# Performance work log

Hardware: AMD Instinct MI355X
Metric: run time of the kernel (lower is better)

## Reference

```python
import jax, jax.numpy as jnp
import numpy as np

N_G, E_G = 50000, 800000
N_S, E_S = 10000, 160000
NF = 64
B = 8

def _w(key, shape):
    fan_in = shape[-1]
    return jax.random.normal(key, shape, dtype=jnp.float32) / np.sqrt(fan_in)

def setup_inputs() -> dict:
    key = jax.random.key(0)
    ks = jax.random.split(key, 40)
    inp = {
        "graph_x": jax.random.normal(ks[0], (N_G, NF), dtype=jnp.float32),
        "subgraph_x": jax.random.normal(ks[1], (N_S, NF), dtype=jnp.float32),
        "point": jax.random.normal(ks[2], (B, NF), dtype=jnp.float32),
        "graph_edge_index": jax.random.randint(ks[3], (2, E_G), 0, N_G),
        "graph_batch": jnp.sort(jax.random.randint(ks[4], (N_G,), 0, B)),
        "subgraph_edge_index": jax.random.randint(ks[5], (2, E_S), 0, N_S),
        "subgraph_batch": jnp.sort(jax.random.randint(ks[6], (N_S,), 0, B)),
    }
    # GraphConv params per branch: channel sizes 64->128->256->192
    dims = [(2 * NF, NF), (4 * NF, 2 * NF), (3 * NF, 4 * NF)]
    i = 7
    for pre in ("g", "s"):
        for li, (o, c) in enumerate(dims, start=1):
            inp[f"{pre}W{li}r"] = _w(ks[i], (o, c)); i += 1  # lin_rel (aggregated)
            inp[f"{pre}W{li}n"] = _w(ks[i], (o, c)); i += 1  # lin_root (self)
            inp[f"{pre}B{li}"] = jnp.zeros((o,), dtype=jnp.float32)
    inp["l1W"] = _w(ks[i], (600, 3 * NF + 3 * NF + NF)); i += 1
    inp["l1b"] = jnp.zeros((600,), dtype=jnp.float32)
    inp["l2W"] = _w(ks[i], (256, 600)); i += 1
    inp["l2b"] = jnp.zeros((256,), dtype=jnp.float32)
    inp["l3W"] = _w(ks[i], (NF, 256)); i += 1
    inp["l3b"] = jnp.zeros((NF,), dtype=jnp.float32)
    return inp

def _graph_conv(x, src, dst, Wr, Wn, b, n_nodes):
    # PyG GraphConv: out_i = Wr @ sum_{j->i} x_j + Wn @ x_i + b
    agg = jax.ops.segment_sum(x[src], dst, num_segments=n_nodes)
    return agg @ Wr.T + x @ Wn.T + b

def _scatter_mean(x, seg, num_segments):
    s = jax.ops.segment_sum(x, seg, num_segments=num_segments)
    cnt = jax.ops.segment_sum(jnp.ones((x.shape[0],), x.dtype), seg, num_segments=num_segments)
    return s / jnp.maximum(cnt, 1.0)[:, None]

def _branch(x, edge_index, batch, params, n_nodes):
    src, dst = edge_index[0], edge_index[1]
    for (Wr, Wn, b) in params:
        x = jax.nn.elu(_graph_conv(x, src, dst, Wr, Wn, b, n_nodes))
    return _scatter_mean(x, batch, B)

def reference(graph_x, subgraph_x, point,
              gW1r, gW1n, gB1, gW2r, gW2n, gB2, gW3r, gW3n, gB3,
              sW1r, sW1n, sB1, sW2r, sW2n, sB2, sW3r, sW3n, sB3,
              l1W, l1b, l2W, l2b, l3W, l3b,
              graph_edge_index, graph_batch, subgraph_edge_index, subgraph_batch):
    x1 = _branch(graph_x, graph_edge_index, graph_batch,
                 [(gW1r, gW1n, gB1), (gW2r, gW2n, gB2), (gW3r, gW3n, gB3)], N_G)
    x2 = _branch(subgraph_x, subgraph_edge_index, subgraph_batch,
                 [(sW1r, sW1n, sB1), (sW2r, sW2n, sB2), (sW3r, sW3n, sB3)], N_S)
    x = jnp.concatenate([x1, x2, point], axis=-1)  # [B, 448]
    x = jax.nn.relu(x @ l1W.T + l1b)
    x = jax.nn.relu(x @ l2W.T + l2b)
    return x @ l3W.T + l3b  # [B, 64]
```

## Files before the change

kernel.cpp:

```cpp
#include <hip/hip_runtime.h>
#include <cmath>

typedef __attribute__((ext_vector_type(8))) short short8;
typedef __attribute__((ext_vector_type(4))) short shortx4;
typedef __attribute__((ext_vector_type(4))) float floatx4;
typedef __attribute__((ext_vector_type(2))) float floatx2;
typedef __attribute__((ext_vector_type(4))) int intx4;
typedef __attribute__((ext_vector_type(2))) int intx2;

#define N_G 50000
#define E_G 800000
#define N_S 10000
#define E_S 160000
#define NT (N_G + N_S)
#define ET (E_G + E_S)
#define BATCH 8
#define STRIDE 64
#define FPASS 8

__device__ __forceinline__ float b2f(short s) {
    unsigned u = ((unsigned)(unsigned short)s) << 16;
    return __builtin_bit_cast(float, u);
}
__device__ __forceinline__ short f2b(float f) {
    unsigned u = __builtin_bit_cast(unsigned, f);
    u += 0x7FFF + ((u >> 16) & 1);
    return (short)(u >> 16);
}
__device__ __forceinline__ short8 fp8x8_to_bf16(intx2 w) {
    floatx2 f0 = __builtin_amdgcn_cvt_pk_f32_fp8(w[0], false);
    floatx2 f1 = __builtin_amdgcn_cvt_pk_f32_fp8(w[0], true);
    floatx2 f2 = __builtin_amdgcn_cvt_pk_f32_fp8(w[1], false);
    floatx2 f3 = __builtin_amdgcn_cvt_pk_f32_fp8(w[1], true);
    short8 r;
    r[0]=f2b(f0[0]); r[1]=f2b(f0[1]); r[2]=f2b(f1[0]); r[3]=f2b(f1[1]);
    r[4]=f2b(f2[0]); r[5]=f2b(f2[1]); r[6]=f2b(f3[0]); r[7]=f2b(f3[1]);
    return r;
}

struct RepArgs { const float* Wr[6]; const float* Wn[6]; short* dst[6]; int cin[6]; int nk[6]; int groups[6]; };
__global__ void init_kernel(const float* __restrict__ gx, const float* __restrict__ sx,
                            unsigned char* __restrict__ X0_8,
                            int* __restrict__ dcount, float* __restrict__ pooled,
                            const int* __restrict__ g_batch, const int* __restrict__ s_batch,
                            int* __restrict__ starts, RepArgs ra, int total_groups) {
    int t = blockIdx.x * blockDim.x + threadIdx.x;
    if (t < NT * 16) {
        size_t e = (size_t)t * 4;
        const float* src = (e < (size_t)N_G * 64) ? (gx + e) : (sx + (e - (size_t)N_G * 64));
        floatx4 v = *(const floatx4*)src;
        int w8 = 0;
        w8 = __builtin_amdgcn_cvt_pk_fp8_f32(v[0], v[1], w8, false);
        w8 = __builtin_amdgcn_cvt_pk_fp8_f32(v[2], v[3], w8, true);
        *(unsigned int*)(X0_8 + e) = (unsigned int)w8;
    }
    if (t < NT) dcount[t] = 0;
    if (t < 16 * 192) pooled[t] = 0.f;
    if (t <= 16) {
        int b = t;
        if (b == 16) { starts[16] = NT; }
        else {
            int key, n, base;
            const int* arr;
            if (b < 8) { arr = g_batch; n = N_G; key = b; base = 0; }
            else       { arr = s_batch; n = N_S; key = b - 8; base = N_G; }
            int lo = 0, hi = n;
            while (lo < hi) { int mid = (lo + hi) >> 1; if (arr[mid] < key) lo = mid + 1; else hi = mid; }
            starts[b] = base + lo;
        }
    }
    if (t < total_groups) {
        int seg = 0, off = t;
        while (seg < 5 && off >= ra.groups[seg]) { off -= ra.groups[seg]; ++seg; }
        int CIN = ra.cin[seg], NK = ra.nk[seg];
        int lane = off & 63;
        int rest = off >> 6;
        int tt = rest % NK;
        int ot = rest / NK;
        int o = ot * 16 + (lane & 15);
        int kk = tt * 32 + (lane >> 4) * 8;
        const float* src = (kk < CIN) ? (ra.Wr[seg] + (size_t)o * CIN + kk)
                                      : (ra.Wn[seg] + (size_t)o * CIN + (kk - CIN));
        floatx4 u0 = *(const floatx4*)src;
        floatx4 u1 = *(const floatx4*)(src + 4);
        short8 d;
        d[0]=f2b(u0[0]); d[1]=f2b(u0[1]); d[2]=f2b(u0[2]); d[3]=f2b(u0[3]);
        d[4]=f2b(u1[0]); d[5]=f2b(u1[1]); d[6]=f2b(u1[2]); d[7]=f2b(u1[3]);
        *(short8*)(ra.dst[seg] + (size_t)off * 8) = d;
    }
}

__global__ void fill_kernel(const int* __restrict__ g_ei, const int* __restrict__ s_ei,
                            int* __restrict__ dcount, int* __restrict__ csr) {
    int pass = blockIdx.x & (FPASS - 1);
    int lb   = blockIdx.x >> 3;
    int t = lb * blockDim.x + threadIdx.x;
    if (t >= ET) return;
    int dst;
    if (t < E_G) dst = g_ei[E_G + t];
    else         dst = s_ei[E_S + (t - E_G)] + N_G;
    int lo = pass * (NT / FPASS);
    int hi = lo + (NT / FPASS);
    if (dst < lo || dst >= hi) return;
    int src;
    if (t < E_G) src = g_ei[t];
    else         src = s_ei[t - E_G] + N_G;
    int slot = atomicAdd(&dcount[dst], 1);
    if (slot < STRIDE) csr[(size_t)dst * STRIDE + slot] = src;
}

template<int C>
__global__ void agg8_kernel(const unsigned char* __restrict__ x8, const int* __restrict__ dcount,
                            const int* __restrict__ csr, short* __restrict__ out) {
    constexpr int C16 = C / 16;
    int t = blockIdx.x * blockDim.x + threadIdx.x;
    if (t >= NT * C16) return;
    int node = t / C16;
    int ch   = t % C16;
    int e0 = node * STRIDE;
    int e1 = e0 + min(dcount[node], STRIDE);
    float acc[16];
    #pragma unroll
    for (int j = 0; j < 16; ++j) acc[j] = 0.f;
    for (int e = e0; e < e1; ++e) {
        int s = csr[e];
        intx4 w = *(const intx4*)(x8 + (size_t)s * C + ch * 16);
        #pragma unroll
        for (int q = 0; q < 4; ++q) {
            floatx2 f0 = __builtin_amdgcn_cvt_pk_f32_fp8(w[q], false);
            floatx2 f1 = __builtin_amdgcn_cvt_pk_f32_fp8(w[q], true);
            acc[q * 4 + 0] += f0[0];
            acc[q * 4 + 1] += f0[1];
            acc[q * 4 + 2] += f1[0];
            acc[q * 4 + 3] += f1[1];
        }
    }
    short8 o0, o1;
    #pragma unroll
    for (int j = 0; j < 8; ++j) { o0[j] = f2b(acc[j]); o1[j] = f2b(acc[8 + j]); }
    short8* q = (short8*)(out + (size_t)node * C + ch * 16);
    q[0] = o0; q[1] = o1;
}

template<int CIN, int COUT, bool POOL>
__global__ __launch_bounds__(256) void gemm_elu_kernel(
        const short* __restrict__ A1, const unsigned char* __restrict__ A2_8,
        const short* __restrict__ gWF, const short* __restrict__ sWF,
        const float* __restrict__ gB, const float* __restrict__ sB,
        unsigned char* __restrict__ out8,
        float* __restrict__ pooled, const int* __restrict__ starts) {
    constexpr int NK  = CIN / 16;
    constexpr int NOT = COUT / 16;
    constexpr int TILE_SH = NK * 512;
    constexpr int MAX_SH = 16384;
    constexpr int CHUNK_OT = (NOT * TILE_SH <= MAX_SH) ? NOT : (MAX_SH / TILE_SH);
    static_assert(NOT % CHUNK_OT == 0, "chunk must divide NOT");
    constexpr int CH_SH = CHUNK_OT * TILE_SH;
    __shared__ short lds[CH_SH];

    int wave = threadIdx.x >> 6;
    int lane = threadIdx.x & 63;
    int tile0 = blockIdx.x << 2;
    int myTile = tile0 + wave;
    bool active = myTile < (NT / 16);
    int tileC = active ? myTile : (NT / 16 - 1);
    int r0 = tileC * 16;
    bool sub = (r0 >= N_G);
    const short* WF = sub ? sWF : gWF;
    const float* bias = sub ? sB : gB;
    int id = lane & 15, quad = lane >> 4;
    int arow = r0 + id;
    short8 a[NK];
    #pragma unroll
    for (int t = 0; t < NK; ++t) {
        int kk = t * 32 + quad * 8;
        if (kk < CIN) {
            a[t] = *(const short8*)(A1 + (size_t)arow * CIN + kk);
        } else {
            intx2 w = *(const intx2*)(A2_8 + (size_t)arow * CIN + (kk - CIN));
            a[t] = fp8x8_to_bf16(w);
        }
    }
    int seg0 = 0, seg1 = 0;
    if (POOL) {
        while (seg0 < 15 && starts[seg0 + 1] <= r0) ++seg0;
        seg1 = seg0;
        while (seg1 < 15 && starts[seg1 + 1] <= r0 + 15) ++seg1;
    }

    constexpr int BTILE = N_G / 16;
    int lastTile = min(tile0 + 3, NT / 16 - 1);
    bool mixed = (tile0 < BTILE) && (lastTile >= BTILE);

    auto epilogue = [&](int ot, floatx4 acc) {
        int o = ot * 16 + id;
        float bv = bias[o];
        float vr[4];
        #pragma unroll
        for (int r = 0; r < 4; ++r) {
            float v = acc[r] + bv;
            vr[r] = (v > 0.f) ? v : (expf(v) - 1.f);
        }
        if (!active) return;
        if (!POOL) {
            #pragma unroll
            for (int r = 0; r < 4; ++r) {
                int nrow = r0 + quad * 4 + r;
                int w8 = __builtin_amdgcn_cvt_pk_fp8_f32(vr[r], vr[r], 0, false);
                out8[(size_t)nrow * COUT + o] = (unsigned char)(w8 & 0xFF);
            }
        } else if (seg0 == seg1) {
            float vsum = vr[0] + vr[1] + vr[2] + vr[3];
            vsum += __shfl_down(vsum, 32, 64);
            vsum += __shfl_down(vsum, 16, 64);
            if (lane < 16) atomicAdd(&pooled[seg0 * 192 + o], vsum);
        } else {
            #pragma unroll
            for (int r = 0; r < 4; ++r) {
                int nrow = r0 + quad * 4 + r;
                int sg = seg0;
                while (sg < seg1 && starts[sg + 1] <= nrow) ++sg;
                atomicAdd(&pooled[sg * 192 + o], vr[r]);
            }
        }
    };

    if (!mixed) {
        for (int c0 = 0; c0 < NOT; c0 += CHUNK_OT) {
            const short* src = WF + (size_t)c0 * TILE_SH;
            #pragma unroll 4
            for (int i = threadIdx.x * 8; i < CH_SH; i += 256 * 8) {
                *(short8*)&lds[i] = *(const short8*)&src[i];
            }
            __syncthreads();
            #pragma unroll
            for (int otl = 0; otl < CHUNK_OT; ++otl) {
                floatx4 acc = {0.f, 0.f, 0.f, 0.f};
                const short* wp = &lds[otl * TILE_SH + lane * 8];
                #pragma unroll
                for (int t = 0; t < NK; ++t) {
                    short8 b = *(const short8*)(wp + t * 512);
                    acc = __builtin_amdgcn_mfma_f32_16x16x32_bf16(a[t], b, acc, 0, 0, 0);
                }
                epilogue(c0 + otl, acc);
            }
            __syncthreads();
        }
    } else {
        for (int ot = 0; ot < NOT; ++ot) {
            floatx4 acc = {0.f, 0.f, 0.f, 0.f};
            const short* wp = WF + (((size_t)ot * NK) * 64 + lane) * 8;
            #pragma unroll
            for (int t = 0; t < NK; ++t) {
                short8 b = *(const short8*)(wp + (size_t)t * 64 * 8);
                acc = __builtin_amdgcn_mfma_f32_16x16x32_bf16(a[t], b, acc, 0, 0, 0);
            }
            epilogue(ot, acc);
        }
    }
}

__global__ __launch_bounds__(256) void mlp1_kernel(
        const float* __restrict__ pooled, const int* __restrict__ starts,
        const float* __restrict__ point, const float* __restrict__ W,
        const float* __restrict__ bias, float* __restrict__ out) {
    int wave = (blockIdx.x * blockDim.x + threadIdx.x) >> 6;
    int lane = threadIdx.x & 63;
    if (wave >= BATCH * 600) return;
    int b = wave / 600, o = wave % 600;
    float invg = 1.f / (float)max(starts[b + 1] - starts[b], 1);
    float invs = 1.f / (float)max(starts[9 + b] - starts[8 + b], 1);
    const float* w = W + (size_t)o * 448;
    float acc = 0.f;
    for (int i = lane; i < 448; i += 64) {
        float x;
        if (i < 192)      x = pooled[b * 192 + i] * invg;
        else if (i < 384) x = pooled[(8 + b) * 192 + (i - 192)] * invs;
        else              x = point[b * 64 + (i - 384)];
        acc += x * w[i];
    }
    #pragma unroll
    for (int off = 32; off > 0; off >>= 1) acc += __shfl_down(acc, off, 64);
    if (lane == 0) out[wave] = fmaxf(acc + bias[o], 0.f);
}

__global__ __launch_bounds__(256) void dense_wave_kernel(
        const float* __restrict__ in, const float* __restrict__ W,
        const float* __restrict__ bias, float* __restrict__ out,
        int I, int O, int relu) {
    int wave = (blockIdx.x * blockDim.x + threadIdx.x) >> 6;
    int lane = threadIdx.x & 63;
    if (wave >= BATCH * O) return;
    int b = wave / O, o = wave % O;
    const float* x = in + (size_t)b * I;
    const float* w = W + (size_t)o * I;
    float acc = 0.f;
    for (int i = lane; i < I; i += 64) acc += x[i] * w[i];
    #pragma unroll
    for (int off = 32; off > 0; off >>= 1) acc += __shfl_down(acc, off, 64);
    if (lane == 0) {
        acc += bias[o];
        if (relu) acc = fmaxf(acc, 0.f);
        out[wave] = acc;
    }
}

extern "C" void kernel_launch(void* const* d_in, const int* in_sizes, int n_in,
                              void* d_out, int out_size, void* d_ws, size_t ws_size,
                              hipStream_t stream) {
    const float* graph_x = (const float*)d_in[0];
    const float* sub_x   = (const float*)d_in[1];
    const float* point   = (const float*)d_in[2];
    const int*   g_ei    = (const int*)d_in[3];
    const int*   g_batch = (const int*)d_in[4];
    const int*   s_ei    = (const int*)d_in[5];
    const int*   s_batch = (const int*)d_in[6];
    const float* gB1=(const float*)d_in[9],  *gB2=(const float*)d_in[12], *gB3=(const float*)d_in[15];
    const float* sB1=(const float*)d_in[18], *sB2=(const float*)d_in[21], *sB3=(const float*)d_in[24];
    const float* l1W=(const float*)d_in[25], *l1b=(const float*)d_in[26];
    const float* l2W=(const float*)d_in[27], *l2b=(const float*)d_in[28];
    const float* l3W=(const float*)d_in[29], *l3b=(const float*)d_in[30];

    char* ws = (char*)d_ws;
    size_t off = 0;
    auto alloc = [&](size_t bytes) -> char* {
        char* p = ws + off;
        off = (off + bytes + 255) & ~(size_t)255;
        return p;
    };
    int* dcount = (int*)alloc((size_t)NT * 4);
    int* csr = (int*)alloc((size_t)NT * STRIDE * 4);

    const int fsz[3] = {128 * 2 * 64, 256 * 2 * 128, 192 * 2 * 256};
    short* wfrag = (short*)alloc((size_t)(fsz[0] + fsz[1] + fsz[2]) * 2 * 2);
    short* gWF[3], *sWF[3];
    { size_t o2 = 0;
      for (int l = 0; l < 3; ++l) { gWF[l] = wfrag + o2; o2 += fsz[l]; }
      for (int l = 0; l < 3; ++l) { sWF[l] = wfrag + o2; o2 += fsz[l]; } }

    unsigned char* X0_8 = (unsigned char*)alloc((size_t)NT * 64);
    short* agg = (short*)alloc((size_t)NT * 256 * 2);
    unsigned char* h1_8 = (unsigned char*)alloc((size_t)NT * 128);
    unsigned char* h2_8 = (unsigned char*)alloc((size_t)NT * 256);

    float* pooled = (float*)alloc(16 * 192 * 4);
    int* starts = (int*)alloc(17 * 4);
    float* mlp_h1 = (float*)alloc(BATCH * 600 * 4);
    float* mlp_h2 = (float*)alloc(BATCH * 256 * 4);

    RepArgs ra;
    const int cin_l[3] = {64, 128, 256};
    const int nk_l[3]  = {4, 8, 16};
    const int not_l[3] = {8, 16, 12};
    const int wr_idx[6] = {7, 10, 13, 16, 19, 22};
    int total_groups = 0;
    for (int s = 0; s < 6; ++s) {
        int l = s % 3;
        ra.Wr[s] = (const float*)d_in[wr_idx[s]];
        ra.Wn[s] = (const float*)d_in[wr_idx[s] + 1];
        ra.dst[s] = (s < 3) ? gWF[l] : sWF[l];
        ra.cin[s] = cin_l[l];
        ra.nk[s] = nk_l[l];
        ra.groups[s] = not_l[l] * nk_l[l] * 64;
        total_groups += ra.groups[s];
    }

    init_kernel<<<(NT * 16 + 255) / 256, 256, 0, stream>>>(graph_x, sub_x, X0_8, dcount,
                                                           pooled, g_batch, s_batch, starts,
                                                           ra, total_groups);

    fill_kernel<<<((ET + 255) / 256) * FPASS, 256, 0, stream>>>(g_ei, s_ei, dcount, csr);

    constexpr int NW = NT / 16;
    const int gemm_blocks = (NW + 3) / 4;

    agg8_kernel<64><<<(NT * 4 + 255) / 256, 256, 0, stream>>>(X0_8, dcount, csr, agg);
    gemm_elu_kernel<64, 128, false><<<gemm_blocks, 256, 0, stream>>>(
        agg, X0_8, gWF[0], sWF[0], gB1, sB1, h1_8, nullptr, nullptr);
    agg8_kernel<128><<<(NT * 8 + 255) / 256, 256, 0, stream>>>(h1_8, dcount, csr, agg);
    gemm_elu_kernel<128, 256, false><<<gemm_blocks, 256, 0, stream>>>(
        agg, h1_8, gWF[1], sWF[1], gB2, sB2, h2_8, nullptr, nullptr);
    agg8_kernel<256><<<(NT * 16 + 255) / 256, 256, 0, stream>>>(h2_8, dcount, csr, agg);
    gemm_elu_kernel<256, 192, true><<<gemm_blocks, 256, 0, stream>>>(
        agg, h2_8, gWF[2], sWF[2], gB3, sB3, nullptr, pooled, starts);

    mlp1_kernel<<<(BATCH * 600 + 3) / 4, 256, 0, stream>>>(pooled, starts, point, l1W, l1b, mlp_h1);
    dense_wave_kernel<<<(BATCH * 256 + 3) / 4, 256, 0, stream>>>(mlp_h1, l2W, l2b, mlp_h2, 600, 256, 1);
    dense_wave_kernel<<<(BATCH * 64 + 3) / 4, 256, 0, stream>>>(mlp_h2, l3W, l3b, (float*)d_out, 256, 64, 0);
}
```

Measured before the change: 369.5 us.

## Process two row tiles per wave and double-buffer weight chunks via direct LDS loads

Each wave now computes two 16-row tiles, so every weight fragment read from LDS feeds two MFMAs, and each block covers 8 tiles instead of 4. Weight chunks are staged with global_load_lds into a double buffer, so the next chunk is prefetched while the current one is being computed, and one barrier per chunk is dropped. The ELU uses the fast __expf. In exchange, register pressure goes up and only half as many blocks are launched, which may reduce occupancy and latency hiding.

```diff
diff --git a/kernel.cpp b/kernel.cpp
--- a/kernel.cpp
+++ b/kernel.cpp
@@ -36,6 +36,11 @@
     r[0]=f2b(f0[0]); r[1]=f2b(f0[1]); r[2]=f2b(f1[0]); r[3]=f2b(f1[1]);
     r[4]=f2b(f2[0]); r[5]=f2b(f2[1]); r[6]=f2b(f3[0]); r[7]=f2b(f3[1]);
     return r;
+}
+__device__ __forceinline__ void gload_lds16(const void* g, void* l) {
+    __builtin_amdgcn_global_load_lds(
+        (const __attribute__((address_space(1))) unsigned int*)g,
+        (__attribute__((address_space(3))) unsigned int*)l, 16, 0, 0);
 }
 
 struct RepArgs { const float* Wr[6]; const float* Wn[6]; short* dst[6]; int cin[6]; int nk[6]; int groups[6]; };
@@ -156,52 +161,69 @@
     constexpr int CHUNK_OT = (NOT * TILE_SH <= MAX_SH) ? NOT : (MAX_SH / TILE_SH);
     static_assert(NOT % CHUNK_OT == 0, "chunk must divide NOT");
     constexpr int CH_SH = CHUNK_OT * TILE_SH;
-    __shared__ short lds[CH_SH];
+    constexpr int NC = NOT / CHUNK_OT;
+    constexpr int NBUF = (NC > 1) ? 2 : 1;
+    constexpr int MROW = 2;
+    constexpr int TPB = 4 * MROW;
+    constexpr int SREG = CH_SH / 2048;
+    constexpr int NTILE = NT / 16;
+    __shared__ short lds[NBUF][CH_SH];
 
     int wave = threadIdx.x >> 6;
     int lane = threadIdx.x & 63;
-    int tile0 = blockIdx.x << 2;
-    int myTile = tile0 + wave;
-    bool active = myTile < (NT / 16);
-    int tileC = active ? myTile : (NT / 16 - 1);
-    int r0 = tileC * 16;
-    bool sub = (r0 >= N_G);
-    const short* WF = sub ? sWF : gWF;
-    const float* bias = sub ? sB : gB;
     int id = lane & 15, quad = lane >> 4;
-    int arow = r0 + id;
-    short8 a[NK];
-    #pragma unroll
-    for (int t = 0; t < NK; ++t) {
-        int kk = t * 32 + quad * 8;
-        if (kk < CIN) {
-            a[t] = *(const short8*)(A1 + (size_t)arow * CIN + kk);
-        } else {
-            intx2 w = *(const intx2*)(A2_8 + (size_t)arow * CIN + (kk - CIN));
-            a[t] = fp8x8_to_bf16(w);
-        }
-    }
-    int seg0 = 0, seg1 = 0;
+    int tile0 = blockIdx.x * TPB;
+
+    int tl[MROW]; bool act[MROW];
+    #pragma unroll
+    for (int m = 0; m < MROW; ++m) {
+        int t = tile0 + wave * MROW + m;
+        act[m] = (t < NTILE);
+        tl[m] = act[m] ? t : (NTILE - 1);
+    }
+    short8 a[MROW][NK];
+    #pragma unroll
+    for (int m = 0; m < MROW; ++m) {
+        int arow = tl[m] * 16 + id;
+        #pragma unroll
+        for (int t = 0; t < NK; ++t) {
+            int kk = t * 32 + quad * 8;
+            if (kk < CIN) {
+                a[m][t] = *(const short8*)(A1 + (size_t)arow * CIN + kk);
+            } else {
+                intx2 w = *(const intx2*)(A2_8 + (size_t)arow * CIN + (kk - CIN));
+                a[m][t] = fp8x8_to_bf16(w);
+            }
+        }
+    }
+    int seg0[MROW], seg1[MROW];
     if (POOL) {
-        while (seg0 < 15 && starts[seg0 + 1] <= r0) ++seg0;
-        seg1 = seg0;
-        while (seg1 < 15 && starts[seg1 + 1] <= r0 + 15) ++seg1;
+        #pragma unroll
+        for (int m = 0; m < MROW; ++m) {
+            int r0 = tl[m] * 16;
+            int s0 = 0;
+            while (s0 < 15 && starts[s0 + 1] <= r0) ++s0;
+            int s1 = s0;
+            while (s1 < 15 && starts[s1 + 1] <= r0 + 15) ++s1;
+            seg0[m] = s0; seg1[m] = s1;
+        }
     }
 
     constexpr int BTILE = N_G / 16;
-    int lastTile = min(tile0 + 3, NT / 16 - 1);
+    int lastTile = min(tile0 + TPB - 1, NTILE - 1);
     bool mixed = (tile0 < BTILE) && (lastTile >= BTILE);
 
-    auto epilogue = [&](int ot, floatx4 acc) {
+    auto epilogue = [&](int ot, int m, const float* bias, floatx4 acc) {
+        if (!act[m]) return;
         int o = ot * 16 + id;
         float bv = bias[o];
+        int r0 = tl[m] * 16;
         float vr[4];
         #pragma unroll
         for (int r = 0; r < 4; ++r) {
             float v = acc[r] + bv;
-            vr[r] = (v > 0.f) ? v : (expf(v) - 1.f);
-        }
-        if (!active) return;
+            vr[r] = (v > 0.f) ? v : (__expf(v) - 1.f);
+        }
         if (!POOL) {
             #pragma unroll
             for (int r = 0; r < 4; ++r) {
@@ -209,53 +231,72 @@
                 int w8 = __builtin_amdgcn_cvt_pk_fp8_f32(vr[r], vr[r], 0, false);
                 out8[(size_t)nrow * COUT + o] = (unsigned char)(w8 & 0xFF);
             }
-        } else if (seg0 == seg1) {
+        } else if (seg0[m] == seg1[m]) {
             float vsum = vr[0] + vr[1] + vr[2] + vr[3];
             vsum += __shfl_down(vsum, 32, 64);
             vsum += __shfl_down(vsum, 16, 64);
-            if (lane < 16) atomicAdd(&pooled[seg0 * 192 + o], vsum);
+            if (lane < 16) atomicAdd(&pooled[seg0[m] * 192 + o], vsum);
         } else {
             #pragma unroll
             for (int r = 0; r < 4; ++r) {
                 int nrow = r0 + quad * 4 + r;
-                int sg = seg0;
-                while (sg < seg1 && starts[sg + 1] <= nrow) ++sg;
+                int sg = seg0[m];
+                while (sg < seg1[m] && starts[sg + 1] <= nrow) ++sg;
                 atomicAdd(&pooled[sg * 192 + o], vr[r]);
             }
         }
     };
 
     if (!mixed) {
-        for (int c0 = 0; c0 < NOT; c0 += CHUNK_OT) {
-            const short* src = WF + (size_t)c0 * TILE_SH;
-            #pragma unroll 4
-            for (int i = threadIdx.x * 8; i < CH_SH; i += 256 * 8) {
-                *(short8*)&lds[i] = *(const short8*)&src[i];
-            }
-            __syncthreads();
+        bool sub = (tile0 * 16 >= N_G);
+        const short* WF = sub ? sWF : gWF;
+        const float* bias = sub ? sB : gB;
+        auto issue_stage = [&](int c, int buf) {
+            const short* src = WF + (size_t)c * CH_SH + threadIdx.x * 8;
+            short* dst = &lds[buf][threadIdx.x * 8];
+            #pragma unroll
+            for (int i = 0; i < SREG; ++i)
+                gload_lds16(src + i * 2048, dst + i * 2048);
+        };
+        issue_stage(0, 0);
+        __syncthreads();
+        for (int c = 0; c < NC; ++c) {
+            if (c + 1 < NC) issue_stage(c + 1, (c + 1) & 1);
+            const short* base = &lds[c & (NBUF - 1)][lane * 8];
             #pragma unroll
             for (int otl = 0; otl < CHUNK_OT; ++otl) {
-                floatx4 acc = {0.f, 0.f, 0.f, 0.f};
-                const short* wp = &lds[otl * TILE_SH + lane * 8];
+                floatx4 acc[MROW];
+                #pragma unroll
+                for (int m = 0; m < MROW; ++m) acc[m] = floatx4{0.f, 0.f, 0.f, 0.f};
                 #pragma unroll
                 for (int t = 0; t < NK; ++t) {
-                    short8 b = *(const short8*)(wp + t * 512);
-                    acc = __builtin_amdgcn_mfma_f32_16x16x32_bf16(a[t], b, acc, 0, 0, 0);
+                    short8 b = *(const short8*)(base + otl * TILE_SH + t * 512);
+                    #pragma unroll
+                    for (int m = 0; m < MROW; ++m)
+                        acc[m] = __builtin_amdgcn_mfma_f32_16x16x32_bf16(a[m][t], b, acc[m], 0, 0, 0);
                 }
-                epilogue(c0 + otl, acc);
+                #pragma unroll
+                for (int m = 0; m < MROW; ++m)
+                    epilogue(c * CHUNK_OT + otl, m, bias, acc[m]);
             }
-            __syncthreads();
+            if (c + 1 < NC) __syncthreads();
         }
     } else {
-        for (int ot = 0; ot < NOT; ++ot) {
-            floatx4 acc = {0.f, 0.f, 0.f, 0.f};
-            const short* wp = WF + (((size_t)ot * NK) * 64 + lane) * 8;
-            #pragma unroll
-            for (int t = 0; t < NK; ++t) {
-                short8 b = *(const short8*)(wp + (size_t)t * 64 * 8);
-                acc = __builtin_amdgcn_mfma_f32_16x16x32_bf16(a[t], b, acc, 0, 0, 0);
+        #pragma unroll
+        for (int m = 0; m < MROW; ++m) {
+            bool sub = (tl[m] * 16 >= N_G);
+            const short* WF = sub ? sWF : gWF;
+            const float* bias = sub ? sB : gB;
+            for (int ot = 0; ot < NOT; ++ot) {
+                floatx4 acc = {0.f, 0.f, 0.f, 0.f};
+                const short* wp = WF + (((size_t)ot * NK) * 64 + lane) * 8;
+                #pragma unroll
+                for (int t = 0; t < NK; ++t) {
+                    short8 b = *(const short8*)(wp + (size_t)t * 512);
+                    acc = __builtin_amdgcn_mfma_f32_16x16x32_bf16(a[m][t], b, acc, 0, 0, 0);
+                }
+                epilogue(ot, m, bias, acc);
             }
-            epilogue(ot, acc);
         }
     }
 }
@@ -371,8 +412,8 @@
 
     fill_kernel<<<((ET + 255) / 256) * FPASS, 256, 0, stream>>>(g_ei, s_ei, dcount, csr);
 
-    constexpr int NW = NT / 16;
-    const int gemm_blocks = (NW + 3) / 4;
+    constexpr int NTILE = NT / 16;
+    const int gemm_blocks = (NTILE + 7) / 8;
 
     agg8_kernel<64><<<(NT * 4 + 255) / 256, 256, 0, stream>>>(X0_8, dcount, csr, agg);
     gemm_elu_kernel<64, 128, false><<<gemm_blocks, 256, 0, stream>>>(
```

Measured after the change: 374.0 us. Within noise of the previous version (+1.2%).
